# Performance work log

Hardware: AMD Instinct MI355X
Metric: run time of the kernel (lower is better)

The kernel has to match this reference:

```python
import jax, jax.numpy as jnp
import numpy as np

B, S, D, H, DFF = 2, 2048, 1024, 16, 4096
DK = D // H
EPS = 1e-5


def layer_norm(x, gamma, beta, eps=EPS):
    mu = jnp.mean(x, axis=-1, keepdims=True)
    var = jnp.mean(jnp.square(x - mu), axis=-1, keepdims=True)
    return (x - mu) * jax.lax.rsqrt(var + eps) * gamma + beta


def setup_inputs() -> dict:
    key = jax.random.key(0)
    ks = jax.random.split(key, 12)
    s_d = 1.0 / np.sqrt(D)
    s_f = 1.0 / np.sqrt(DFF)
    return {
        "x": jax.random.normal(ks[0], (B, S, D), jnp.float32),
        # per-head QKV projections stacked: [H, D, DK]
        "Wq": jax.random.normal(ks[1], (H, D, DK), jnp.float32) * s_d,
        "bq": jnp.zeros((H, DK), jnp.float32),
        "Wk": jax.random.normal(ks[2], (H, D, DK), jnp.float32) * s_d,
        "bk": jnp.zeros((H, DK), jnp.float32),
        "Wv": jax.random.normal(ks[3], (H, D, DK), jnp.float32) * s_d,
        "bv": jnp.zeros((H, DK), jnp.float32),
        "Wo": jax.random.normal(ks[4], (D, D), jnp.float32) * s_d,
        "bo": jnp.zeros((D,), jnp.float32),
        "W1": jax.random.normal(ks[5], (D, DFF), jnp.float32) * s_d,
        "b1": jnp.zeros((DFF,), jnp.float32),
        "W2": jax.random.normal(ks[6], (DFF, D), jnp.float32) * s_f,
        "b2": jnp.zeros((D,), jnp.float32),
        "ln1_g": jnp.ones((D,), jnp.float32),
        "ln1_b": jnp.zeros((D,), jnp.float32),
        "ln2_g": jnp.ones((D,), jnp.float32),
        "ln2_b": jnp.zeros((D,), jnp.float32),
    }


def reference(x, Wq, bq, Wk, bk, Wv, bv, Wo, bo, W1, b1, W2, b2,
              ln1_g, ln1_b, ln2_g, ln2_b):
    # --- residual 1: pre-norm multi-head self-attention (mask unused, dropout=eval) ---
    h = layer_norm(x, ln1_g, ln1_b)                      # [B,S,D]
    q = jnp.einsum('bsd,hdk->bhsk', h, Wq) + bq[:, None, :]
    k = jnp.einsum('bsd,hdk->bhsk', h, Wk) + bk[:, None, :]
    v = jnp.einsum('bsd,hdk->bhsk', h, Wv) + bv[:, None, :]
    scores = jnp.einsum('bhsk,bhtk->bhst', q, k) / np.sqrt(DK)  # [B,H,S,S]
    w = jax.nn.softmax(scores, axis=-1)
    ctx = jnp.einsum('bhst,bhtk->bhsk', w, v)            # [B,H,S,DK]
    # concat heads along feature dim -> [B,S,D]
    ctx = jnp.transpose(ctx, (0, 2, 1, 3)).reshape(B, S, D)
    attn_out = ctx @ Wo + bo
    x = x + attn_out
    # --- residual 2: pre-norm feed-forward ---
    h2 = layer_norm(x, ln2_g, ln2_b)
    ff = jax.nn.relu(h2 @ W1 + b1) @ W2 + b2
    return x + ff
```

## Files before the change

### kernel.cpp

```cpp
#include <hip/hip_runtime.h>

#define B_   2
#define S_   2048
#define D_   1024
#define H_   16
#define DK_  64
#define DFF_ 4096
#define NT_  (B_*S_)
#define QS_  3072

using u16 = unsigned short;
typedef __attribute__((ext_vector_type(8))) short bf16x8;
typedef __attribute__((ext_vector_type(4))) float f32x4;
typedef __attribute__((ext_vector_type(4))) u16  u16x4;

__device__ __forceinline__ float bf2f(u16 h) {
  union { unsigned u; float f; } c; c.u = ((unsigned)h) << 16; return c.f;
}
__device__ __forceinline__ u16 f2bf(float f) {
  union { float f; unsigned u; } c; c.f = f;
  unsigned u = c.u;
  return (u16)((u + 0x7fffu + ((u >> 16) & 1u)) >> 16);
}
__device__ __forceinline__ u16 f2bf_up(float f) {
  union { float f; unsigned u; } c; c.f = f;
  return (u16)((c.u + 0x8000u) >> 16);
}

__device__ __forceinline__ void load_lds16(const void* g, void* l) {
  __builtin_amdgcn_global_load_lds(
      (const __attribute__((address_space(1))) unsigned int*)g,
      (__attribute__((address_space(3))) unsigned int*)l, 16, 0, 0);
}

__device__ __forceinline__ void store_out(u16* p, float v)   { *p = f2bf(v); }
__device__ __forceinline__ void store_out(float* p, float v) { *p = v; }

__global__ __launch_bounds__(256) void ln_kernel(
    const float* __restrict__ x, const float* __restrict__ g,
    const float* __restrict__ bt, u16* __restrict__ o)
{
  const int row = blockIdx.x, t = threadIdx.x;
  const float4 xv = *(const float4*)(x + (size_t)row * D_ + t * 4);
  float f[4] = {xv.x, xv.y, xv.z, xv.w};
  float sum = f[0] + f[1] + f[2] + f[3];
  float sq  = f[0]*f[0] + f[1]*f[1] + f[2]*f[2] + f[3]*f[3];
#pragma unroll
  for (int d = 32; d >= 1; d >>= 1) {
    sum += __shfl_down(sum, d);
    sq  += __shfl_down(sq, d);
  }
  __shared__ float red[8];
  const int lane = t & 63, wid = t >> 6;
  if (lane == 0) { red[wid] = sum; red[wid + 4] = sq; }
  __syncthreads();
  sum = red[0] + red[1] + red[2] + red[3];
  sq  = red[4] + red[5] + red[6] + red[7];
  const float mu   = sum * (1.0f / D_);
  const float var  = sq * (1.0f / D_) - mu * mu;
  const float rstd = rsqrtf(var + 1e-5f);
  const float4 gv = *(const float4*)(g  + t * 4);
  const float4 bv = *(const float4*)(bt + t * 4);
  u16x4 ov;
  ov[0] = f2bf((f[0] - mu) * rstd * gv.x + bv.x);
  ov[1] = f2bf((f[1] - mu) * rstd * gv.y + bv.y);
  ov[2] = f2bf((f[2] - mu) * rstd * gv.z + bv.z);
  ov[3] = f2bf((f[3] - mu) * rstd * gv.w + bv.w);
  *(u16x4*)(o + (size_t)row * D_ + t * 4) = ov;
}

__global__ __launch_bounds__(256) void transpose_w(
    const float* __restrict__ Wo, const float* __restrict__ W1,
    const float* __restrict__ W2, u16* __restrict__ woT,
    u16* __restrict__ w1T, u16* __restrict__ w2T)
{
  __shared__ float tile[32][33];
  int t = blockIdx.x;
  const float* in; u16* out; int R, C;
  if (t < 1024)      { in = Wo; out = woT; R = 1024; C = 1024; }
  else if (t < 5120) { in = W1; out = w1T; R = 1024; C = 4096; t -= 1024; }
  else               { in = W2; out = w2T; R = 4096; C = 1024; t -= 5120; }
  const int tilesX = C >> 5;
  const int c0 = (t % tilesX) * 32, r0 = (t / tilesX) * 32;
  const int tx = threadIdx.x & 31, ty = threadIdx.x >> 5;
#pragma unroll
  for (int i = 0; i < 32; i += 8)
    tile[ty + i][tx] = in[(size_t)(r0 + ty + i) * C + c0 + tx];
  __syncthreads();
#pragma unroll
  for (int i = 0; i < 32; i += 8)
    out[(size_t)(c0 + ty + i) * R + r0 + tx] = f2bf(tile[tx][ty + i]);
}

__global__ __launch_bounds__(256) void transpose_qkv(
    const float* __restrict__ Wq, const float* __restrict__ Wk,
    const float* __restrict__ Wv, u16* __restrict__ out)
{
  __shared__ float tile[32][33];
  const int z = blockIdx.z;
  const int which = z >> 4, h = z & 15;
  const float* ip = (which == 0 ? Wq : which == 1 ? Wk : Wv) + (size_t)h * 1024 * 64;
  u16* op = out + ((size_t)which * 1024 + h * 64) * 1024;
  const float sc = (which == 0) ? 0.125f : 1.0f;
  const int c0 = blockIdx.x * 32, r0 = blockIdx.y * 32;
  const int tx = threadIdx.x & 31, ty = threadIdx.x >> 5;
#pragma unroll
  for (int i = 0; i < 32; i += 8)
    tile[ty + i][tx] = ip[(size_t)(r0 + ty + i) * 64 + c0 + tx];
  __syncthreads();
#pragma unroll
  for (int i = 0; i < 32; i += 8)
    op[(size_t)(c0 + ty + i) * 1024 + r0 + tx] = f2bf(tile[tx][ty + i] * sc);
}

__global__ __launch_bounds__(256) void pack_kv(
    const u16* __restrict__ qkv, u16* __restrict__ kt, u16* __restrict__ vt)
{
  __shared__ u16 tile[32][72];
  const int z = blockIdx.y;
  const int b = z >> 4, h = z & 15;
  const int t0 = blockIdx.x * 32;
  const int tid = threadIdx.x;
  const int row = tid >> 3, sub = tid & 7;

  const u16* src = qkv + (size_t)(b * S_ + t0 + row) * QS_ + h * DK_ + sub * 8;
  *(bf16x8*)(kt + ((size_t)z * S_ + t0 + row) * 64 + sub * 8) =
      *(const bf16x8*)(src + 1024);
  *(bf16x8*)&tile[row][sub * 8] = *(const bf16x8*)(src + 2048);
  __syncthreads();

  const int d = tid >> 2, tc = (tid & 3) * 8;
  bf16x8 val;
#pragma unroll
  for (int j = 0; j < 8; ++j) val[j] = (short)tile[tc + j][d];
  *(bf16x8*)(vt + ((size_t)z * 64 + d) * S_ + t0 + tc) = val;
}

template <typename OT, int KK>
__global__ __launch_bounds__(512, 1) void gemm256(
    const u16* __restrict__ A, const u16* __restrict__ Bt,
    const float* __restrict__ bias, const float* __restrict__ biasB,
    const float* __restrict__ biasC, OT* __restrict__ C,
    int M, int N, int do_relu)
{
  constexpr int NK = KK / 32;
  __shared__ u16 lA[4][256 * 32];
  __shared__ u16 lB[4][256 * 32];
  const int tid = threadIdx.x, lane = tid & 63, wid = tid >> 6;
  const int wr = wid >> 2, wc = wid & 3;

  const int nbx = gridDim.x;
  int bid = blockIdx.y * nbx + blockIdx.x;
  const int cpx = (nbx * gridDim.y) >> 3;
  bid = (bid & 7) * cpx + (bid >> 3);
  const int row0 = (bid / nbx) * 256, col0 = (bid % nbx) * 256;

  const int c0 = tid,       sr0 = c0 >> 2, q0 = ((c0 & 3) ^ (((sr0 >> 3) & 1) << 1)) * 8;
  const int c1 = tid + 512, sr1 = c1 >> 2, q1 = ((c1 & 3) ^ (((sr1 >> 3) & 1) << 1)) * 8;
  const u16* As0 = A  + (size_t)(row0 + sr0) * KK + q0;
  const u16* As1 = A  + (size_t)(row0 + sr1) * KK + q1;
  const u16* Bs0 = Bt + (size_t)(col0 + sr0) * KK + q0;
  const u16* Bs1 = Bt + (size_t)(col0 + sr1) * KK + q1;

  f32x4 acc[8][4] = {};
  const int lrow = lane & 15, kcol = (lane >> 4) * 8;

#pragma unroll
  for (int t = 0; t < 3; ++t) {
    load_lds16(As0 + t * 32, &lA[t][c0 * 8]);
    load_lds16(Bs0 + t * 32, &lB[t][c0 * 8]);
    load_lds16(As1 + t * 32, &lA[t][c1 * 8]);
    load_lds16(Bs1 + t * 32, &lB[t][c1 * 8]);
  }
  asm volatile("s_waitcnt vmcnt(8)" ::: "memory");
  __builtin_amdgcn_sched_barrier(0);
  __builtin_amdgcn_s_barrier();

#pragma unroll 4
  for (int j = 0; j < NK; ++j) {
    const int b = j & 3;
    const u16* la = lA[b];
    const u16* lb = lB[b];
    bf16x8 af[4], bfr[4];

#pragma unroll
    for (int m = 0; m < 4; ++m) {
      const int row = wr * 128 + m * 16 + lrow;
      af[m] = *(const bf16x8*)&la[row * 32 + (kcol ^ (((row >> 3) & 1) << 4))];
    }
#pragma unroll
    for (int n = 0; n < 4; ++n) {
      const int row = wc * 64 + n * 16 + lrow;
      bfr[n] = *(const bf16x8*)&lb[row * 32 + (kcol ^ (((row >> 3) & 1) << 4))];
    }
    if (j + 3 < NK) {
      const int bb = (j + 3) & 3;
      load_lds16(As0 + (j + 3) * 32, &lA[bb][c0 * 8]);
      load_lds16(Bs0 + (j + 3) * 32, &lB[bb][c0 * 8]);
    }
    __builtin_amdgcn_s_setprio(1);
#pragma unroll
    for (int m = 0; m < 4; ++m)
#pragma unroll
      for (int n = 0; n < 4; ++n)
        acc[m][n] = __builtin_amdgcn_mfma_f32_16x16x32_bf16(af[m], bfr[n], acc[m][n], 0, 0, 0);
    __builtin_amdgcn_s_setprio(0);

#pragma unroll
    for (int m = 0; m < 4; ++m) {
      const int row = wr * 128 + (m + 4) * 16 + lrow;
      af[m] = *(const bf16x8*)&la[row * 32 + (kcol ^ (((row >> 3) & 1) << 4))];
    }
    if (j + 3 < NK) {
      const int bb = (j + 3) & 3;
      load_lds16(As1 + (j + 3) * 32, &lA[bb][c1 * 8]);
      load_lds16(Bs1 + (j + 3) * 32, &lB[bb][c1 * 8]);
    }
    __builtin_amdgcn_s_setprio(1);
#pragma unroll
    for (int m = 0; m < 4; ++m)
#pragma unroll
      for (int n = 0; n < 4; ++n)
        acc[m + 4][n] = __builtin_amdgcn_mfma_f32_16x16x32_bf16(af[m], bfr[n], acc[m + 4][n], 0, 0, 0);
    __builtin_amdgcn_s_setprio(0);
    if (j + 3 < NK)      { asm volatile("s_waitcnt vmcnt(8)" ::: "memory"); }
    else if (j + 2 < NK) { asm volatile("s_waitcnt vmcnt(4)" ::: "memory"); }
    else if (j + 1 < NK) { asm volatile("s_waitcnt vmcnt(0)" ::: "memory"); }
    __builtin_amdgcn_sched_barrier(0);
    __builtin_amdgcn_s_barrier();
  }

#pragma unroll
  for (int m = 0; m < 8; ++m)
#pragma unroll
    for (int n = 0; n < 4; ++n) {
      const int rbase = row0 + wr*128 + m*16 + ((lane >> 4) << 2);
      const int c     = col0 + wc*64 + n*16 + (lane & 15);
      float bv = 0.f;
      if (biasC)      bv = c < 1024 ? bias[c] * 0.125f
                         : (c < 2048 ? biasB[c - 1024] : biasC[c - 2048]);
      else if (bias)  bv = bias[c];
#pragma unroll
      for (int r = 0; r < 4; ++r) {
        float vv = acc[m][n][r] + bv;
        if (do_relu) vv = vv > 0.f ? vv : 0.f;
        store_out(&C[(size_t)(rbase + r) * N + c], vv);
      }
    }
}

template <int KK>
__global__ __launch_bounds__(512, 1) void gemm256pk(
    const u16* __restrict__ A, const u16* __restrict__ Bt,
    u16* __restrict__ P, int M, int N, int Ktot)
{
  constexpr int NK = KK / 32;
  __shared__ u16 lA[4][256 * 32];
  __shared__ u16 lB[4][256 * 32];
  const int tid = threadIdx.x, lane = tid & 63, wid = tid >> 6;
  const int wr = wid >> 2, wc = wid & 3;

  const int nbx = gridDim.x;
  int bid = blockIdx.y * nbx + blockIdx.x;
  const int cpx = (nbx * gridDim.y) >> 3;
  bid = (bid & 7) * cpx + (bid >> 3);
  const int row0 = (bid / nbx) * 256, col0 = (bid % nbx) * 256;
  const int kb = blockIdx.z * KK;

  const int c0 = tid,       sr0 = c0 >> 2, q0 = ((c0 & 3) ^ (((sr0 >> 3) & 1) << 1)) * 8;
  const int c1 = tid + 512, sr1 = c1 >> 2, q1 = ((c1 & 3) ^ (((sr1 >> 3) & 1) << 1)) * 8;
  const u16* As0 = A  + (size_t)(row0 + sr0) * Ktot + kb + q0;
  const u16* As1 = A  + (size_t)(row0 + sr1) * Ktot + kb + q1;
  const u16* Bs0 = Bt + (size_t)(col0 + sr0) * Ktot + kb + q0;
  const u16* Bs1 = Bt + (size_t)(col0 + sr1) * Ktot + kb + q1;

  f32x4 acc[8][4] = {};
  const int lrow = lane & 15, kcol = (lane >> 4) * 8;

#pragma unroll
  for (int t = 0; t < 3; ++t) {
    load_lds16(As0 + t * 32, &lA[t][c0 * 8]);
    load_lds16(Bs0 + t * 32, &lB[t][c0 * 8]);
    load_lds16(As1 + t * 32, &lA[t][c1 * 8]);
    load_lds16(Bs1 + t * 32, &lB[t][c1 * 8]);
  }
  asm volatile("s_waitcnt vmcnt(8)" ::: "memory");
  __builtin_amdgcn_sched_barrier(0);
  __builtin_amdgcn_s_barrier();

#pragma unroll 4
  for (int j = 0; j < NK; ++j) {
    const int b = j & 3;
    const u16* la = lA[b];
    const u16* lb = lB[b];
    bf16x8 af[4], bfr[4];

#pragma unroll
    for (int m = 0; m < 4; ++m) {
      const int row = wr * 128 + m * 16 + lrow;
      af[m] = *(const bf16x8*)&la[row * 32 + (kcol ^ (((row >> 3) & 1) << 4))];
    }
#pragma unroll
    for (int n = 0; n < 4; ++n) {
      const int row = wc * 64 + n * 16 + lrow;
      bfr[n] = *(const bf16x8*)&lb[row * 32 + (kcol ^ (((row >> 3) & 1) << 4))];
    }
    if (j + 3 < NK) {
      const int bb = (j + 3) & 3;
      load_lds16(As0 + (j + 3) * 32, &lA[bb][c0 * 8]);
      load_lds16(Bs0 + (j + 3) * 32, &lB[bb][c0 * 8]);
    }
    __builtin_amdgcn_s_setprio(1);
#pragma unroll
    for (int m = 0; m < 4; ++m)
#pragma unroll
      for (int n = 0; n < 4; ++n)
        acc[m][n] = __builtin_amdgcn_mfma_f32_16x16x32_bf16(af[m], bfr[n], acc[m][n], 0, 0, 0);
    __builtin_amdgcn_s_setprio(0);

#pragma unroll
    for (int m = 0; m < 4; ++m) {
      const int row = wr * 128 + (m + 4) * 16 + lrow;
      af[m] = *(const bf16x8*)&la[row * 32 + (kcol ^ (((row >> 3) & 1) << 4))];
    }
    if (j + 3 < NK) {
      const int bb = (j + 3) & 3;
      load_lds16(As1 + (j + 3) * 32, &lA[bb][c1 * 8]);
      load_lds16(Bs1 + (j + 3) * 32, &lB[bb][c1 * 8]);
    }
    __builtin_amdgcn_s_setprio(1);
#pragma unroll
    for (int m = 0; m < 4; ++m)
#pragma unroll
      for (int n = 0; n < 4; ++n)
        acc[m + 4][n] = __builtin_amdgcn_mfma_f32_16x16x32_bf16(af[m], bfr[n], acc[m + 4][n], 0, 0, 0);
    __builtin_amdgcn_s_setprio(0);
    if (j + 3 < NK)      { asm volatile("s_waitcnt vmcnt(8)" ::: "memory"); }
    else if (j + 2 < NK) { asm volatile("s_waitcnt vmcnt(4)" ::: "memory"); }
    else if (j + 1 < NK) { asm volatile("s_waitcnt vmcnt(0)" ::: "memory"); }
    __builtin_amdgcn_sched_barrier(0);
    __builtin_amdgcn_s_barrier();
  }

  u16* Pz = P + (size_t)blockIdx.z * M * N;
#pragma unroll
  for (int m = 0; m < 8; ++m)
#pragma unroll
    for (int n = 0; n < 4; ++n) {
      const int rbase = row0 + wr*128 + m*16 + ((lane >> 4) << 2);
      const int c     = col0 + wc*64 + n*16 + (lane & 15);
#pragma unroll
      for (int r = 0; r < 4; ++r)
        Pz[(size_t)(rbase + r) * N + c] = f2bf(acc[m][n][r]);
    }
}

template <typename OT>
__global__ __launch_bounds__(256) void gemm_bt64(
    const u16* __restrict__ A, const u16* __restrict__ Bt,
    const float* __restrict__ bias, const float* __restrict__ res,
    OT* __restrict__ C, int M, int N, int K, int do_relu)
{
  __shared__ u16 lA[2][128 * 32];
  __shared__ u16 lB[2][64 * 32];
  const int tid = threadIdx.x, lane = tid & 63, wid = tid >> 6;

  const int nbx = gridDim.x;
  int bid = blockIdx.y * nbx + blockIdx.x;
  const int cpx = (nbx * gridDim.y) >> 3;
  bid = (bid & 7) * cpx + (bid >> 3);
  const int row0 = (bid / nbx) * 128, col0 = (bid % nbx) * 64;

  f32x4 acc[2][4] = {};

  const int cc0 = tid, cc1 = tid + 256;
  const int r0 = cc0 >> 2, s0 = cc0 & 3;
  const int r1 = cc1 >> 2, s1 = cc1 & 3;
  const int ko0 = (s0 ^ ((r0 >> 1) & 3)) * 8;
  const int ko1 = (s1 ^ ((r1 >> 1) & 3)) * 8;

#define GST64(bf, k0)                                                         \
  {                                                                           \
    load_lds16(A  + (size_t)(row0 + r0) * K + (k0) + ko0, &lA[bf][cc0 * 8]);  \
    load_lds16(A  + (size_t)(row0 + r1) * K + (k0) + ko1, &lA[bf][cc1 * 8]);  \
    load_lds16(Bt + (size_t)(col0 + r0) * K + (k0) + ko0, &lB[bf][cc0 * 8]);  \
  }

  const int nk = K >> 5;
  GST64(0, 0);
  int cur = 0;
  for (int t = 0; t < nk; ++t) {
    __syncthreads();
    if (t + 1 < nk) GST64(cur ^ 1, (t + 1) * 32);
    bf16x8 af[2], bfr[4];
#pragma unroll
    for (int m = 0; m < 2; ++m) {
      const int row = wid * 32 + m * 16 + (lane & 15);
      af[m] = *(const bf16x8*)&lA[cur][row * 32 + (((lane >> 4) ^ ((row >> 1) & 3)) * 8)];
    }
#pragma unroll
    for (int n = 0; n < 4; ++n) {
      const int row = n * 16 + (lane & 15);
      bfr[n] = *(const bf16x8*)&lB[cur][row * 32 + (((lane >> 4) ^ ((row >> 1) & 3)) * 8)];
    }
#pragma unroll
    for (int m = 0; m < 2; ++m)
#pragma unroll
      for (int n = 0; n < 4; ++n)
        acc[m][n] = __builtin_amdgcn_mfma_f32_16x16x32_bf16(af[m], bfr[n], acc[m][n], 0, 0, 0);
    cur ^= 1;
  }
#undef GST64

#pragma unroll
  for (int m = 0; m < 2; ++m)
#pragma unroll
    for (int n = 0; n < 4; ++n) {
      const int rbase = row0 + wid*32 + m*16 + ((lane >> 4) << 2);
      const int c     = col0 + n*16 + (lane & 15);
      const float bv  = bias ? bias[c] : 0.f;
#pragma unroll
      for (int r = 0; r < 4; ++r) {
        const int rr = rbase + r;
        float vv = acc[m][n][r] + bv;
        if (res) vv += res[(size_t)rr * N + c];
        if (do_relu) vv = vv > 0.f ? vv : 0.f;
        store_out(&C[(size_t)rr * N + c], vv);
      }
    }
}

__global__ __launch_bounds__(256) void ffr_reduce4(
    const u16* __restrict__ P, const float* __restrict__ x1,
    const float* __restrict__ b2, float* __restrict__ out)
{
  const size_t i = (size_t)blockIdx.x * 256 + threadIdx.x;
  const size_t M4 = (size_t)NT_ * D_;
  const float4 r  = ((const float4*)x1)[i];
  const float4 bb = ((const float4*)b2)[i & 255];
  float o0 = r.x + bb.x, o1 = r.y + bb.y, o2 = r.z + bb.z, o3 = r.w + bb.w;
#pragma unroll
  for (int z = 0; z < 4; ++z) {
    const u16x4 p = *(const u16x4*)(P + z * M4 + i * 4);
    o0 += bf2f(p[0]); o1 += bf2f(p[1]); o2 += bf2f(p[2]); o3 += bf2f(p[3]);
  }
  float4 o; o.x = o0; o.y = o1; o.z = o2; o.w = o3;
  ((float4*)out)[i] = o;
}

__global__ __launch_bounds__(512) void attn_kernel(
    const u16* __restrict__ QKV, const u16* __restrict__ Kt,
    const u16* __restrict__ Vt, u16* __restrict__ O)
{
  __shared__ u16 lK[2][64 * 64];
  __shared__ u16 lV[2][64 * 64];
  __shared__ u16 lP[128 * 64];

  const int tid = threadIdx.x, lane = tid & 63, wid = tid >> 6;
  const int g  = (blockIdx.x & 7) * 64 + (blockIdx.x >> 3);
  const int qt = g & 15, h = (g >> 4) & 15, b = g >> 8;
  const int z  = b * H_ + h;

  const u16* Qp  = QKV + (size_t)(b * S_ + qt * 128) * QS_ + h * DK_;
  const u16* Kpb = Kt + (size_t)z * S_ * 64;
  const u16* Vb  = Vt + (size_t)z * DK_ * S_;

  bf16x8 qf[2];
  {
    const int qr = wid * 16 + (lane & 15);
    qf[0] = *(const bf16x8*)(Qp + (size_t)qr * QS_ + (lane >> 4) * 8);
    qf[1] = *(const bf16x8*)(Qp + (size_t)qr * QS_ + 32 + (lane >> 4) * 8);
  }

  const bf16x8 vone = {16256,16256,16256,16256,16256,16256,16256,16256};

#define STAGE_KV(bf, kt_)                                                     \
  {                                                                           \
    const u16* Kp = Kpb + (size_t)(kt_) * 64 * 64;                            \
    const u16* Vp = Vb + (size_t)(kt_) * 64;                                  \
    const int c = tid, r = c >> 3, sub = c & 7;                               \
    load_lds16(Kp + r * 64 + ((sub ^ (r & 7)) * 8), &lK[bf][c * 8]);          \
    load_lds16(Vp + (size_t)r * S_ + ((sub ^ (r & 7)) * 8), &lV[bf][c * 8]);  \
  }

  float m_run = -1e30f;
  f32x4 l_acc = {};
  f32x4 o_acc[4] = {};

  STAGE_KV(0, 0);
  int cur = 0;

  for (int kt = 0; kt < S_ / 64; ++kt) {
    __syncthreads();
    if (kt + 1 < S_ / 64) STAGE_KV(cur ^ 1, kt + 1);

    f32x4 s[4];
    __builtin_amdgcn_s_setprio(1);
#pragma unroll
    for (int kf = 0; kf < 4; ++kf) {
      const int row = kf * 16 + (lane & 15);
      const int i0 = (row * 64 + (lane >> 4) * 8)      ^ ((row & 7) << 3);
      const int i1 = (row * 64 + 32 + (lane >> 4) * 8) ^ ((row & 7) << 3);
      bf16x8 k0 = *(const bf16x8*)&lK[cur][i0];
      bf16x8 k1 = *(const bf16x8*)&lK[cur][i1];
      f32x4 sc = {};
      sc = __builtin_amdgcn_mfma_f32_16x16x32_bf16(k0, qf[0], sc, 0, 0, 0);
      sc = __builtin_amdgcn_mfma_f32_16x16x32_bf16(k1, qf[1], sc, 0, 0, 0);
      s[kf] = sc;
    }
    __builtin_amdgcn_s_setprio(0);

    float t0 = fmaxf(fmaxf(s[0][0], s[0][1]), fmaxf(s[0][2], s[0][3]));
    float t1 = fmaxf(fmaxf(s[1][0], s[1][1]), fmaxf(s[1][2], s[1][3]));
    float t2 = fmaxf(fmaxf(s[2][0], s[2][1]), fmaxf(s[2][2], s[2][3]));
    float t3 = fmaxf(fmaxf(s[3][0], s[3][1]), fmaxf(s[3][2], s[3][3]));
    float pmax = fmaxf(fmaxf(t0, t1), fmaxf(t2, t3));
    pmax = fmaxf(pmax, __shfl_xor(pmax, 16));
    pmax = fmaxf(pmax, __shfl_xor(pmax, 32));

    const bool grow = pmax > m_run + 8.0f;
    const float mnew = grow ? pmax : m_run;
    if (__any(grow)) {
      const float scale = __expf(m_run - mnew);
#pragma unroll
      for (int r = 0; r < 4; ++r) {
        const float sr = __shfl(scale, (lane >> 4) * 4 + r);
        l_acc[r] *= sr;
#pragma unroll
        for (int nf = 0; nf < 4; ++nf) o_acc[nf][r] *= sr;
      }
    }
    m_run = mnew;

    const int prow = wid * 16 + (lane & 15);
#pragma unroll
    for (int kf = 0; kf < 4; ++kf) {
      u16x4 pk;
#pragma unroll
      for (int r = 0; r < 4; ++r) pk[r] = f2bf_up(__expf(s[kf][r] - m_run));
      const int idx = (prow * 64 + kf * 16 + (lane >> 4) * 4) ^ ((prow & 7) << 3);
      *(u16x4*)&lP[idx] = pk;
    }
    asm volatile("s_waitcnt lgkmcnt(0)" ::: "memory");
    __builtin_amdgcn_sched_barrier(0);

    bf16x8 pa0 = *(const bf16x8*)&lP[(prow * 64 + (lane >> 4) * 8)      ^ ((prow & 7) << 3)];
    bf16x8 pa1 = *(const bf16x8*)&lP[(prow * 64 + 32 + (lane >> 4) * 8) ^ ((prow & 7) << 3)];
    __builtin_amdgcn_s_setprio(1);
    l_acc = __builtin_amdgcn_mfma_f32_16x16x32_bf16(pa0, vone, l_acc, 0, 0, 0);
    l_acc = __builtin_amdgcn_mfma_f32_16x16x32_bf16(pa1, vone, l_acc, 0, 0, 0);
#pragma unroll
    for (int nf = 0; nf < 4; ++nf) {
      const int vrow = nf * 16 + (lane & 15);
      bf16x8 v0 = *(const bf16x8*)&lV[cur][(vrow * 64 + (lane >> 4) * 8)      ^ ((vrow & 7) << 3)];
      bf16x8 v1 = *(const bf16x8*)&lV[cur][(vrow * 64 + 32 + (lane >> 4) * 8) ^ ((vrow & 7) << 3)];
      o_acc[nf] = __builtin_amdgcn_mfma_f32_16x16x32_bf16(pa0, v0, o_acc[nf], 0, 0, 0);
      o_acc[nf] = __builtin_amdgcn_mfma_f32_16x16x32_bf16(pa1, v1, o_acc[nf], 0, 0, 0);
    }
    __builtin_amdgcn_s_setprio(0);
    cur ^= 1;
  }

#pragma unroll
  for (int nf = 0; nf < 4; ++nf)
#pragma unroll
    for (int r = 0; r < 4; ++r) {
      const int qrow = qt * 128 + wid * 16 + (lane >> 4) * 4 + r;
      const int col  = h * DK_ + nf * 16 + (lane & 15);
      O[(size_t)(b * S_ + qrow) * D_ + col] = f2bf(o_acc[nf][r] / l_acc[r]);
    }
}

extern "C" void kernel_launch(void* const* d_in, const int* in_sizes, int n_in,
                              void* d_out, int out_size, void* d_ws, size_t ws_size,
                              hipStream_t stream)
{
  const float* x   = (const float*)d_in[0];
  const float* Wq  = (const float*)d_in[1];
  const float* bq  = (const float*)d_in[2];
  const float* Wk  = (const float*)d_in[3];
  const float* bk  = (const float*)d_in[4];
  const float* Wv  = (const float*)d_in[5];
  const float* bv  = (const float*)d_in[6];
  const float* Wo  = (const float*)d_in[7];
  const float* bo  = (const float*)d_in[8];
  const float* W1  = (const float*)d_in[9];
  const float* b1  = (const float*)d_in[10];
  const float* W2  = (const float*)d_in[11];
  const float* b2  = (const float*)d_in[12];
  const float* g1  = (const float*)d_in[13];
  const float* be1 = (const float*)d_in[14];
  const float* g2  = (const float*)d_in[15];
  const float* be2 = (const float*)d_in[16];
  float* out = (float*)d_out;

  const size_t MB = 1024 * 1024;
  char* base = (char*)d_ws;
  u16*   xn    = (u16*)(base);
  u16*   qkv   = (u16*)(base +  8*MB);
  u16*   ctx   = (u16*)(base + 32*MB);
  float* x1    = (float*)(base + 40*MB);
  u16*   vt    = (u16*)(base + 40*MB);
  u16*   kt    = (u16*)(base + 48*MB);
  u16*   ff1   = (u16*)(base +  8*MB);
  u16*   wqkvT = (u16*)(base + 56*MB);
  u16*   woT   = (u16*)(base + 62*MB);
  u16*   w1T   = (u16*)(base + 64*MB);
  u16*   w2T   = (u16*)(base + 72*MB);
  u16*   pkh   = (u16*)(base + 80*MB);

  const bool splitk = ws_size >= (size_t)112 * MB;

  dim3 blk(256);
  transpose_qkv<<<dim3(2, 32, 48), blk, 0, stream>>>(Wq, Wk, Wv, wqkvT);
  transpose_w<<<dim3(9216), blk, 0, stream>>>(Wo, W1, W2, woT, w1T, w2T);

  ln_kernel<<<NT_, blk, 0, stream>>>(x, g1, be1, xn);

  gemm256<u16, 1024><<<dim3(12, 16), dim3(512), 0, stream>>>(
      xn, wqkvT, bq, bk, bv, qkv, NT_, QS_, 0);

  pack_kv<<<dim3(S_ / 32, B_ * H_), blk, 0, stream>>>(qkv, kt, vt);

  attn_kernel<<<dim3(512), dim3(512), 0, stream>>>(qkv, kt, vt, ctx);

  gemm_bt64<<<dim3(16, 32), blk, 0, stream>>>(ctx, woT, bo, x, x1, NT_, D_, D_, 0);

  ln_kernel<<<NT_, blk, 0, stream>>>(x1, g2, be2, xn);

  gemm256<u16, 1024><<<dim3(16, 16), dim3(512), 0, stream>>>(
      xn, w1T, b1, (const float*)nullptr, (const float*)nullptr, ff1, NT_, DFF_, 1);

  if (splitk) {
    gemm256pk<1024><<<dim3(4, 16, 4), dim3(512), 0, stream>>>(
        ff1, w2T, pkh, NT_, D_, DFF_);
    ffr_reduce4<<<dim3(4096), blk, 0, stream>>>(pkh, x1, b2, out);
  } else {
    gemm_bt64<<<dim3(16, 32), blk, 0, stream>>>(ff1, w2T, b2, x1, out, NT_, D_, DFF_, 0);
  }
}
```

Baseline: 255.1 us.

## Split attention over KV halves with flash-decoding style merge kernel

Each query tile's KV range is split into two halves processed by separate blocks, doubling the grid from 512 to 1024 blocks so more of the CUs stay busy. Partial unnormalized outputs (bf16), row sums and running maxima are written to workspace, and a new merge kernel combines them with log-sum-exp rescaling. This trades extra global traffic, a second launch and bf16 rounding of the partial outputs for higher occupancy and better load balance in the attention stage.

```diff
diff --git a/kernel.cpp b/kernel.cpp
--- a/kernel.cpp
+++ b/kernel.cpp
@@ -448,17 +448,22 @@
   ((float4*)out)[i] = o;
 }
 
+template <int NSPLIT>
 __global__ __launch_bounds__(512) void attn_kernel(
     const u16* __restrict__ QKV, const u16* __restrict__ Kt,
-    const u16* __restrict__ Vt, u16* __restrict__ O)
+    const u16* __restrict__ Vt, u16* __restrict__ O,
+    u16* __restrict__ po, float* __restrict__ pl, float* __restrict__ pm)
 {
   __shared__ u16 lK[2][64 * 64];
   __shared__ u16 lV[2][64 * 64];
   __shared__ u16 lP[128 * 64];
 
   const int tid = threadIdx.x, lane = tid & 63, wid = tid >> 6;
-  const int g  = (blockIdx.x & 7) * 64 + (blockIdx.x >> 3);
-  const int qt = g & 15, h = (g >> 4) & 15, b = g >> 8;
+  const int chunk = 64 * NSPLIT;
+  const int g  = (blockIdx.x & 7) * chunk + (blockIdx.x >> 3);
+  const int half = g % NSPLIT;
+  const int g2 = g / NSPLIT;
+  const int qt = g2 & 15, h = (g2 >> 4) & 15, b = g2 >> 8;
   const int z  = b * H_ + h;
 
   const u16* Qp  = QKV + (size_t)(b * S_ + qt * 128) * QS_ + h * DK_;
@@ -487,12 +492,15 @@
   f32x4 l_acc = {};
   f32x4 o_acc[4] = {};
 
-  STAGE_KV(0, 0);
+  constexpr int NT2 = 32 / NSPLIT;
+  const int ktbase = half * NT2;
+
+  STAGE_KV(0, ktbase);
   int cur = 0;
 
-  for (int kt = 0; kt < S_ / 64; ++kt) {
+  for (int ktl = 0; ktl < NT2; ++ktl) {
     __syncthreads();
-    if (kt + 1 < S_ / 64) STAGE_KV(cur ^ 1, kt + 1);
+    if (ktl + 1 < NT2) STAGE_KV(cur ^ 1, ktbase + ktl + 1);
 
     f32x4 s[4];
     __builtin_amdgcn_s_setprio(1);
@@ -561,14 +569,59 @@
     cur ^= 1;
   }
 
-#pragma unroll
-  for (int nf = 0; nf < 4; ++nf)
-#pragma unroll
-    for (int r = 0; r < 4; ++r) {
-      const int qrow = qt * 128 + wid * 16 + (lane >> 4) * 4 + r;
-      const int col  = h * DK_ + nf * 16 + (lane & 15);
-      O[(size_t)(b * S_ + qrow) * D_ + col] = f2bf(o_acc[nf][r] / l_acc[r]);
-    }
+  const int hi = lane >> 4;
+  if (NSPLIT == 1) {
+#pragma unroll
+    for (int nf = 0; nf < 4; ++nf)
+#pragma unroll
+      for (int r = 0; r < 4; ++r) {
+        const int qrow = qt * 128 + wid * 16 + hi * 4 + r;
+        const int col  = h * DK_ + nf * 16 + (lane & 15);
+        O[(size_t)(b * S_ + qrow) * D_ + col] = f2bf(o_acc[nf][r] / l_acc[r]);
+      }
+  } else {
+#pragma unroll
+    for (int nf = 0; nf < 4; ++nf)
+#pragma unroll
+      for (int r = 0; r < 4; ++r) {
+        const int gtok = b * S_ + qt * 128 + wid * 16 + hi * 4 + r;
+        const int col  = h * DK_ + nf * 16 + (lane & 15);
+        po[((size_t)half * NT_ + gtok) * 1024 + col] = f2bf(o_acc[nf][r]);
+      }
+    if ((lane & 15) == 0) {
+#pragma unroll
+      for (int r = 0; r < 4; ++r) {
+        const int gtok = b * S_ + qt * 128 + wid * 16 + hi * 4 + r;
+        pl[((size_t)half * NT_ + gtok) * 16 + h] = l_acc[r];
+      }
+    }
+    if (lane < 16) {
+      const int gtok = b * S_ + qt * 128 + wid * 16 + lane;
+      pm[((size_t)half * NT_ + gtok) * 16 + h] = m_run;
+    }
+  }
+}
+
+__global__ __launch_bounds__(256) void attn_merge(
+    const u16* __restrict__ po, const float* __restrict__ pl,
+    const float* __restrict__ pm, u16* __restrict__ ctx)
+{
+  const int tok = blockIdx.x, t = threadIdx.x;
+  const int col = t * 4, h = col >> 6;
+  const float m1 = pm[(size_t)tok * 16 + h];
+  const float m2 = pm[((size_t)NT_ + tok) * 16 + h];
+  const float l1 = pl[(size_t)tok * 16 + h];
+  const float l2 = pl[((size_t)NT_ + tok) * 16 + h];
+  const float M  = fmaxf(m1, m2);
+  const float a1 = __expf(m1 - M), a2 = __expf(m2 - M);
+  const float inv = 1.0f / (a1 * l1 + a2 * l2);
+  const u16x4 o1 = *(const u16x4*)(po + (size_t)tok * 1024 + col);
+  const u16x4 o2 = *(const u16x4*)(po + ((size_t)NT_ + tok) * 1024 + col);
+  u16x4 o;
+#pragma unroll
+  for (int j = 0; j < 4; ++j)
+    o[j] = f2bf((a1 * bf2f(o1[j]) + a2 * bf2f(o2[j])) * inv);
+  *(u16x4*)(ctx + (size_t)tok * 1024 + col) = o;
 }
 
 extern "C" void kernel_launch(void* const* d_in, const int* in_sizes, int n_in,
@@ -607,6 +660,9 @@
   u16*   woT   = (u16*)(base + 62*MB);
   u16*   w1T   = (u16*)(base + 64*MB);
   u16*   w2T   = (u16*)(base + 72*MB);
+  u16*   poh   = (u16*)(base + 80*MB);
+  float* plf   = (float*)(base + 96*MB);
+  float* pmf   = (float*)(base + 97*MB);
   u16*   pkh   = (u16*)(base + 80*MB);
 
   const bool splitk = ws_size >= (size_t)112 * MB;
@@ -622,7 +678,14 @@
 
   pack_kv<<<dim3(S_ / 32, B_ * H_), blk, 0, stream>>>(qkv, kt, vt);
 
-  attn_kernel<<<dim3(512), dim3(512), 0, stream>>>(qkv, kt, vt, ctx);
+  if (splitk) {
+    attn_kernel<2><<<dim3(1024), dim3(512), 0, stream>>>(
+        qkv, kt, vt, (u16*)nullptr, poh, plf, pmf);
+    attn_merge<<<dim3(NT_), blk, 0, stream>>>(poh, plf, pmf, ctx);
+  } else {
+    attn_kernel<1><<<dim3(512), dim3(512), 0, stream>>>(
+        qkv, kt, vt, ctx, (u16*)nullptr, (float*)nullptr, (float*)nullptr);
+  }
 
   gemm_bt64<<<dim3(16, 32), blk, 0, stream>>>(ctx, woT, bo, x, x1, NT_, D_, D_, 0);
 
```

Measured after the change: 262.3 us. 1.03x slower.
